# Performance work log

Hardware: AMD Instinct MI355X
Metric: run time of the kernel (lower is better)

The kernel has to match this reference:

```python
import jax, jax.numpy as jnp
import numpy as np

N = 8_000_000
NUM_MOLS = 200_000

def setup_inputs() -> dict:
    key = jax.random.key(0)
    k1, k2 = jax.random.split(key)
    atoms_x = jax.random.normal(k1, (N, 3), dtype=jnp.float32)
    graph_batch = jnp.sort(jax.random.randint(k2, (N,), 0, NUM_MOLS, dtype=jnp.int64))
    return {"atoms_x": atoms_x, "graph_batch": graph_batch, "num_mols": NUM_MOLS}

def reference(atoms_x, graph_batch, num_mols):
    # Per-molecule mean via single-pass segment reduction (replaces O(N*num_mols) mask loop)
    seg_sum = jax.ops.segment_sum(atoms_x, graph_batch, num_segments=num_mols)          # [M, 3]
    counts = jax.ops.segment_sum(jnp.ones((atoms_x.shape[0],), atoms_x.dtype),
                                 graph_batch, num_segments=num_mols)                    # [M]
    mean = seg_sum / jnp.maximum(counts, 1.0)[:, None]                                  # empty mols -> 0 center
    return atoms_x - mean[graph_batch]
```

## Files before the change

kernel.cpp:

```cpp
#include <hip/hip_runtime.h>


static constexpr int TPB   = 64;
static constexpr int CPT   = 16;
static constexpr int CHUNK = TPB * CPT;
static constexpr int SLOTS = 128;

__global__ __launch_bounds__(TPB) void fused_center_kernel(
    const float* __restrict__ x, const int* __restrict__ gb,
    float* __restrict__ out, int n) {
  __shared__ float sums[SLOTS * 4];

  const int lane = threadIdx.x;
  const long long cs = (long long)blockIdx.x * CHUNK;
  const long long ce = (cs + CHUNK < (long long)n) ? cs + CHUNK : (long long)n;
  const int fid = gb[cs];
  const int lid = gb[ce - 1];
  const int span = lid - fid + 1;

  if (span > SLOTS) {
    if (lane == 0) {
      long long i = cs;
      while (i < ce) {
        int id = gb[i];
        long long rs = i; while (rs > 0 && gb[rs - 1] == id) --rs;
        long long re = i; while (re < n && gb[re] == id) ++re;
        float sx = 0.f, sy = 0.f, sz = 0.f;
        for (long long k = rs; k < re; ++k) {
          sx += x[k * 3 + 0]; sy += x[k * 3 + 1]; sz += x[k * 3 + 2];
        }
        float inv = 1.f / (float)(re - rs);
        float mx = sx * inv, my = sy * inv, mz = sz * inv;
        long long we = (re < ce) ? re : ce;
        for (long long k = i; k < we; ++k) {
          out[k * 3 + 0] = x[k * 3 + 0] - mx;
          out[k * 3 + 1] = x[k * 3 + 1] - my;
          out[k * 3 + 2] = x[k * 3 + 2] - mz;
        }
        i = we;
      }
    }
    return;
  }

  const long long base = cs + (long long)lane * CPT;
  const bool full = (base + CPT <= ce);

  float f[CPT * 3];
  int ids[CPT];
  if (full) {
    const float4* xv = reinterpret_cast<const float4*>(x + base * 3);
#pragma unroll
    for (int j = 0; j < CPT * 3 / 4; ++j) {
      float4 v = xv[j];
      f[j * 4 + 0] = v.x; f[j * 4 + 1] = v.y;
      f[j * 4 + 2] = v.z; f[j * 4 + 3] = v.w;
    }
    const int4* gv = reinterpret_cast<const int4*>(gb + base);
#pragma unroll
    for (int j = 0; j < CPT / 4; ++j) {
      int4 g = gv[j];
      ids[j * 4 + 0] = g.x; ids[j * 4 + 1] = g.y;
      ids[j * 4 + 2] = g.z; ids[j * 4 + 3] = g.w;
    }
  }

  for (int i = lane; i < span * 4; i += TPB) sums[i] = 0.f;
  __syncthreads();

  if (full) {
    int cur = ids[0];
    float sx = 0.f, sy = 0.f, sz = 0.f, sc = 0.f;
#pragma unroll
    for (int j = 0; j < CPT; ++j) {
      if (ids[j] != cur) {
        int s = (cur - fid) * 4;
        atomicAdd(&sums[s + 0], sx); atomicAdd(&sums[s + 1], sy);
        atomicAdd(&sums[s + 2], sz); atomicAdd(&sums[s + 3], sc);
        cur = ids[j]; sx = sy = sz = sc = 0.f;
      }
      sx += f[j * 3 + 0]; sy += f[j * 3 + 1]; sz += f[j * 3 + 2]; sc += 1.f;
    }
    {
      int s = (cur - fid) * 4;
      atomicAdd(&sums[s + 0], sx); atomicAdd(&sums[s + 1], sy);
      atomicAdd(&sums[s + 2], sz); atomicAdd(&sums[s + 3], sc);
    }
  } else if (base < ce) {
    for (long long i = base; i < ce; ++i) {
      int s = (gb[i] - fid) * 4;
      atomicAdd(&sums[s + 0], x[i * 3 + 0]);
      atomicAdd(&sums[s + 1], x[i * 3 + 1]);
      atomicAdd(&sums[s + 2], x[i * 3 + 2]);
      atomicAdd(&sums[s + 3], 1.f);
    }
  }

  if (cs > 0) {
    float hx = 0.f, hy = 0.f, hz = 0.f, hc = 0.f;
    long long off = 1 + lane;
    for (;;) {
      long long i = cs - off;
      bool m = (i >= 0) && (gb[i] == fid);
      if (m) {
        hx += x[i * 3 + 0]; hy += x[i * 3 + 1]; hz += x[i * 3 + 2]; hc += 1.f;
      }
      if (__popcll(__ballot(m)) < TPB) break;
      off += TPB;
    }
#pragma unroll
    for (int d = 1; d < 64; d <<= 1) {
      hx += __shfl_xor(hx, d); hy += __shfl_xor(hy, d);
      hz += __shfl_xor(hz, d); hc += __shfl_xor(hc, d);
    }
    if (lane == 0 && hc > 0.f) {
      atomicAdd(&sums[0], hx); atomicAdd(&sums[1], hy);
      atomicAdd(&sums[2], hz); atomicAdd(&sums[3], hc);
    }
  }
  if (ce < (long long)n) {
    float hx = 0.f, hy = 0.f, hz = 0.f, hc = 0.f;
    long long off = (long long)lane;
    for (;;) {
      long long i = ce + off;
      bool m = (i < (long long)n) && (gb[i] == lid);
      if (m) {
        hx += x[i * 3 + 0]; hy += x[i * 3 + 1]; hz += x[i * 3 + 2]; hc += 1.f;
      }
      if (__popcll(__ballot(m)) < TPB) break;
      off += TPB;
    }
#pragma unroll
    for (int d = 1; d < 64; d <<= 1) {
      hx += __shfl_xor(hx, d); hy += __shfl_xor(hy, d);
      hz += __shfl_xor(hz, d); hc += __shfl_xor(hc, d);
    }
    if (lane == 0 && hc > 0.f) {
      int s = (lid - fid) * 4;
      atomicAdd(&sums[s + 0], hx); atomicAdd(&sums[s + 1], hy);
      atomicAdd(&sums[s + 2], hz); atomicAdd(&sums[s + 3], hc);
    }
  }
  __syncthreads();

  for (int s = lane; s < span; s += TPB) {
    float c = sums[s * 4 + 3];
    if (c > 0.f) {
      float inv = 1.f / c;
      sums[s * 4 + 0] *= inv; sums[s * 4 + 1] *= inv; sums[s * 4 + 2] *= inv;
    }
  }
  __syncthreads();

  if (full) {
#pragma unroll
    for (int j = 0; j < CPT; ++j) {
      int s = (ids[j] - fid) * 4;
      f[j * 3 + 0] -= sums[s + 0];
      f[j * 3 + 1] -= sums[s + 1];
      f[j * 3 + 2] -= sums[s + 2];
    }
    float4* ov = reinterpret_cast<float4*>(out + base * 3);
#pragma unroll
    for (int j = 0; j < CPT * 3 / 4; ++j)
      ov[j] = make_float4(f[j * 4 + 0], f[j * 4 + 1],
                          f[j * 4 + 2], f[j * 4 + 3]);
  } else if (base < ce) {
    for (long long i = base; i < ce; ++i) {
      int s = (gb[i] - fid) * 4;
      out[i * 3 + 0] = x[i * 3 + 0] - sums[s + 0];
      out[i * 3 + 1] = x[i * 3 + 1] - sums[s + 1];
      out[i * 3 + 2] = x[i * 3 + 2] - sums[s + 2];
    }
  }
}

extern "C" void kernel_launch(void* const* d_in, const int* in_sizes, int n_in,
                              void* d_out, int out_size, void* d_ws, size_t ws_size,
                              hipStream_t stream) {
  const float* x = (const float*)d_in[0];
  const int* gb = (const int*)d_in[1];
  float* out = (float*)d_out;
  const int n = in_sizes[0] / 3;

  int blocks = (int)(((long long)n + CHUNK - 1) / CHUNK);
  fused_center_kernel<<<blocks, TPB, 0, stream>>>(x, gb, out, n);
}
```

Before: 54.40 us.

## Coalesce chunk loads with strided float4 access and per-element shared atomics

Each thread used to load a contiguous run of 16 atoms. Now the block's whole chunk of coordinates is loaded with lane-strided float4 accesses so each wavefront instruction touches contiguous memory, and the ids are staged in shared memory. The per-thread run-length accumulation is replaced by per-element LDS atomics, with the atom and component worked out from the flat float index, and the output is written back with coalesced float4 stores. This removes the uncoalesced per-thread strided global accesses. In exchange it issues far more shared-memory atomics, roughly one or two per float instead of a few per thread, and these can contend when all atoms fall in the same molecule.

```diff
diff --git a/kernel.cpp b/kernel.cpp
--- a/kernel.cpp
+++ b/kernel.cpp
@@ -1,14 +1,19 @@
 #include <hip/hip_runtime.h>
 
+
+typedef float f32x4 __attribute__((ext_vector_type(4)));
 
 static constexpr int TPB   = 64;
 static constexpr int CPT   = 16;
 static constexpr int CHUNK = TPB * CPT;
+static constexpr int F4PT  = CHUNK * 3 / 4 / TPB;
+static constexpr int I4PT  = CHUNK / 4 / TPB;
 static constexpr int SLOTS = 128;
 
 __global__ __launch_bounds__(TPB) void fused_center_kernel(
     const float* __restrict__ x, const int* __restrict__ gb,
     float* __restrict__ out, int n) {
+  __shared__ alignas(16) int idbuf[CHUNK];
   __shared__ float sums[SLOTS * 4];
 
   const int lane = threadIdx.x;
@@ -43,57 +48,54 @@
     return;
   }
 
-  const long long base = cs + (long long)lane * CPT;
-  const bool full = (base + CPT <= ce);
+  const int na  = (int)(ce - cs);
+  const int nf  = na * 3;
+  const int nf4 = nf / 4;
+  const int ni4 = na / 4;
+  const int nir = na - ni4 * 4;
 
-  float f[CPT * 3];
-  int ids[CPT];
-  if (full) {
-    const float4* xv = reinterpret_cast<const float4*>(x + base * 3);
+  f32x4 xr[F4PT];
+  const f32x4* xv = reinterpret_cast<const f32x4*>(x + cs * 3);
 #pragma unroll
-    for (int j = 0; j < CPT * 3 / 4; ++j) {
-      float4 v = xv[j];
-      f[j * 4 + 0] = v.x; f[j * 4 + 1] = v.y;
-      f[j * 4 + 2] = v.z; f[j * 4 + 3] = v.w;
-    }
-    const int4* gv = reinterpret_cast<const int4*>(gb + base);
+  for (int j = 0; j < F4PT; ++j) {
+    int i4 = j * TPB + lane;
+    xr[j] = (i4 < nf4) ? xv[i4] : (f32x4){0.f, 0.f, 0.f, 0.f};
+  }
+
+  const int4* gv = reinterpret_cast<const int4*>(gb + cs);
 #pragma unroll
-    for (int j = 0; j < CPT / 4; ++j) {
-      int4 g = gv[j];
-      ids[j * 4 + 0] = g.x; ids[j * 4 + 1] = g.y;
-      ids[j * 4 + 2] = g.z; ids[j * 4 + 3] = g.w;
-    }
+  for (int j = 0; j < I4PT; ++j) {
+    int i4 = j * TPB + lane;
+    if (i4 < ni4)
+      reinterpret_cast<int4*>(idbuf)[i4] = gv[i4];
   }
+  if (lane < nir) idbuf[ni4 * 4 + lane] = gb[cs + ni4 * 4 + lane];
 
   for (int i = lane; i < span * 4; i += TPB) sums[i] = 0.f;
   __syncthreads();
 
-  if (full) {
-    int cur = ids[0];
-    float sx = 0.f, sy = 0.f, sz = 0.f, sc = 0.f;
 #pragma unroll
-    for (int j = 0; j < CPT; ++j) {
-      if (ids[j] != cur) {
-        int s = (cur - fid) * 4;
-        atomicAdd(&sums[s + 0], sx); atomicAdd(&sums[s + 1], sy);
-        atomicAdd(&sums[s + 2], sz); atomicAdd(&sums[s + 3], sc);
-        cur = ids[j]; sx = sy = sz = sc = 0.f;
+  for (int j = 0; j < F4PT; ++j) {
+    int i4 = j * TPB + lane;
+    if (i4 < nf4) {
+      int e = i4 * 4;
+      int atom = (int)(((unsigned)e * 0xAAABu) >> 17);
+      int comp = e - atom * 3;
+#pragma unroll
+      for (int c = 0; c < 4; ++c) {
+        int s = (idbuf[atom] - fid) * 4;
+        atomicAdd(&sums[s + comp], xr[j][c]);
+        if (comp == 0) atomicAdd(&sums[s + 3], 1.f);
+        if (++comp == 3) { comp = 0; ++atom; }
       }
-      sx += f[j * 3 + 0]; sy += f[j * 3 + 1]; sz += f[j * 3 + 2]; sc += 1.f;
     }
-    {
-      int s = (cur - fid) * 4;
-      atomicAdd(&sums[s + 0], sx); atomicAdd(&sums[s + 1], sy);
-      atomicAdd(&sums[s + 2], sz); atomicAdd(&sums[s + 3], sc);
-    }
-  } else if (base < ce) {
-    for (long long i = base; i < ce; ++i) {
-      int s = (gb[i] - fid) * 4;
-      atomicAdd(&sums[s + 0], x[i * 3 + 0]);
-      atomicAdd(&sums[s + 1], x[i * 3 + 1]);
-      atomicAdd(&sums[s + 2], x[i * 3 + 2]);
-      atomicAdd(&sums[s + 3], 1.f);
-    }
+  }
+  for (int e = nf4 * 4 + lane; e < nf; e += TPB) {
+    int atom = (int)(((unsigned)e * 0xAAABu) >> 17);
+    int comp = e - atom * 3;
+    int s = (idbuf[atom] - fid) * 4;
+    atomicAdd(&sums[s + comp], x[cs * 3 + e]);
+    if (comp == 0) atomicAdd(&sums[s + 3], 1.f);
   }
 
   if (cs > 0) {
@@ -152,26 +154,29 @@
   }
   __syncthreads();
 
-  if (full) {
+  f32x4* ov = reinterpret_cast<f32x4*>(out + cs * 3);
 #pragma unroll
-    for (int j = 0; j < CPT; ++j) {
-      int s = (ids[j] - fid) * 4;
-      f[j * 3 + 0] -= sums[s + 0];
-      f[j * 3 + 1] -= sums[s + 1];
-      f[j * 3 + 2] -= sums[s + 2];
+  for (int j = 0; j < F4PT; ++j) {
+    int i4 = j * TPB + lane;
+    if (i4 < nf4) {
+      int e = i4 * 4;
+      int atom = (int)(((unsigned)e * 0xAAABu) >> 17);
+      int comp = e - atom * 3;
+      f32x4 o;
+#pragma unroll
+      for (int c = 0; c < 4; ++c) {
+        int s = (idbuf[atom] - fid) * 4;
+        o[c] = xr[j][c] - sums[s + comp];
+        if (++comp == 3) { comp = 0; ++atom; }
+      }
+      ov[i4] = o;
     }
-    float4* ov = reinterpret_cast<float4*>(out + base * 3);
-#pragma unroll
-    for (int j = 0; j < CPT * 3 / 4; ++j)
-      ov[j] = make_float4(f[j * 4 + 0], f[j * 4 + 1],
-                          f[j * 4 + 2], f[j * 4 + 3]);
-  } else if (base < ce) {
-    for (long long i = base; i < ce; ++i) {
-      int s = (gb[i] - fid) * 4;
-      out[i * 3 + 0] = x[i * 3 + 0] - sums[s + 0];
-      out[i * 3 + 1] = x[i * 3 + 1] - sums[s + 1];
-      out[i * 3 + 2] = x[i * 3 + 2] - sums[s + 2];
-    }
+  }
+  for (int e = nf4 * 4 + lane; e < nf; e += TPB) {
+    int atom = (int)(((unsigned)e * 0xAAABu) >> 17);
+    int comp = e - atom * 3;
+    int s = (idbuf[atom] - fid) * 4;
+    out[cs * 3 + e] = x[cs * 3 + e] - sums[s + comp];
   }
 }
 
```

Result: slower. 210.2 us (+286.3%).
